# Kernel tuning notes

Hardware: AMD Instinct MI355X
Metric: run time of the kernel (lower is better)

## Reference

```python
import jax, jax.numpy as jnp
import numpy as np

E = 1024  # embedding_dim
H = 64    # head_size

def setup_inputs() -> dict:
    key = jax.random.key(0)
    k1, k2, k3, k4 = jax.random.split(key, 4)
    x = jax.random.normal(k1, (4, 4096, E), dtype=jnp.float32)
    # nn.Linear(E, H, bias=False) weights have shape [H, E]; y = x @ W.T
    s = 1.0 / np.sqrt(E)
    Wq = jax.random.normal(k2, (H, E), dtype=jnp.float32) * s
    Wk = jax.random.normal(k3, (H, E), dtype=jnp.float32) * s
    Wv = jax.random.normal(k4, (H, E), dtype=jnp.float32) * s
    return {"x": x, "Wq": Wq, "Wk": Wk, "Wv": Wv}

def reference(x, Wq, Wk, Wv):
    B, T, E_ = x.shape
    q = jnp.einsum('bte,he->bth', x, Wq)
    k = jnp.einsum('bte,he->bth', x, Wk)
    v = jnp.einsum('bte,he->bth', x, Wv)
    # NOTE: original scales by sqrt(embedding_dim), not head_size
    scores = jnp.einsum('bqh,bkh->bqk', q, k) / jnp.sqrt(jnp.asarray(E_, x.dtype))
    causal = jnp.tril(jnp.ones((T, T), dtype=bool))
    scores = jnp.where(causal, scores, -jnp.inf)
    weights = jax.nn.softmax(scores, axis=-1)
    return jnp.einsum('bqk,bkh->bqh', weights, v)
```

## Files before the change

### kernel.cpp

```cpp
#include <hip/hip_runtime.h>
#include <stdint.h>

typedef __bf16 bf16x8 __attribute__((ext_vector_type(8)));
typedef float  f32x4  __attribute__((ext_vector_type(4)));

#define E_DIM 1024
#define H_DIM 64
#define T_SEQ 4096
#define B_BAT 4
#define M_TOT (B_BAT * T_SEQ)

__device__ __forceinline__ uint32_t f2bf1(float f) {
    uint32_t u = __float_as_uint(f);
    return (u + 0x7FFFu + ((u >> 16) & 1u)) >> 16;
}
__device__ __forceinline__ uint32_t pk2(float lo, float hi) {
    return f2bf1(lo) | (f2bf1(hi) << 16);
}
__device__ __forceinline__ bf16x8 ldfrag(const ushort* p) {
    return __builtin_bit_cast(bf16x8, *(const uint4*)(p));
}
__device__ __forceinline__ void barrier_lgkm() {
    __builtin_amdgcn_s_waitcnt(0xC07F);
    __builtin_amdgcn_s_barrier();
}

__global__ __launch_bounds__(256) void wcvt(const float* __restrict__ Wq,
                                            const float* __restrict__ Wk,
                                            const float* __restrict__ Wv,
                                            ushort* __restrict__ Wfm) {
    int g = blockIdx.x * 256 + threadIdx.x;
    int n = g >> 7;
    int k8 = g & 127;
    const float* src = (n < 64) ? (Wq + (size_t)n * E_DIM)
                     : (n < 128) ? (Wk + (size_t)(n - 64) * E_DIM)
                     : (Wv + (size_t)(n - 128) * E_DIM);
    float sc = (n < 64) ? 0.03125f : 1.0f;
    float4 a = *(const float4*)(src + k8 * 8);
    float4 b = *(const float4*)(src + k8 * 8 + 4);
    uint4 o;
    o.x = pk2(a.x * sc, a.y * sc); o.y = pk2(a.z * sc, a.w * sc);
    o.z = pk2(b.x * sc, b.y * sc); o.w = pk2(b.z * sc, b.w * sc);
    int s = k8 >> 3, kc = (k8 >> 2) & 1, qd = k8 & 3;
    int nt = n >> 4, lm = n & 15;
    int lane = qd * 16 + lm;
    *(uint4*)(Wfm + (((size_t)(s * 12 + nt) * 2 + kc) * 64 + lane) * 8) = o;
}

__global__ __launch_bounds__(256, 3) void qkv(const float* __restrict__ x,
                                              const ushort* __restrict__ Wfm,
                                              ushort* __restrict__ Qfm,
                                              ushort* __restrict__ Kfm,
                                              ushort* __restrict__ Vfm) {
    __shared__ union {
        ushort a[2][32 * 72];
        struct { ushort c[32 * 136]; ushort vt[64 * 40]; } epi;
    } sm;
    const int tid = threadIdx.x;
    const int w = tid >> 6, l = tid & 63;
    const int lm = l & 15, qd = l >> 4;
    const int m0 = blockIdx.x * 32;

    f32x4 acc[2][3];
#pragma unroll
    for (int r2 = 0; r2 < 2; ++r2)
#pragma unroll
        for (int t = 0; t < 3; ++t) acc[r2][t] = (f32x4){0.f, 0.f, 0.f, 0.f};

    const int srow = tid >> 3, kseg = tid & 7;
    const float* xsrc = x + (size_t)(m0 + srow) * E_DIM + kseg * 8;

    {
        float4 a0 = *(const float4*)xsrc;
        float4 a1 = *(const float4*)(xsrc + 4);
        uint4 u = {pk2(a0.x, a0.y), pk2(a0.z, a0.w), pk2(a1.x, a1.y), pk2(a1.z, a1.w)};
        *(uint4*)(&sm.a[0][srow * 72 + kseg * 8]) = u;
    }
    float4 xn0 = *(const float4*)(xsrc + 64);
    float4 xn1 = *(const float4*)(xsrc + 68);
    __syncthreads();

    for (int s = 0; s < 16; ++s) {
        const int cb = s & 1, nb = cb ^ 1;
        float4 x20 = xn0, x21 = xn1;
        if (s < 14) {
            x20 = *(const float4*)(xsrc + (s + 2) * 64);
            x21 = *(const float4*)(xsrc + (s + 2) * 64 + 4);
        }
        bf16x8 wf[3][2];
#pragma unroll
        for (int t = 0; t < 3; ++t)
#pragma unroll
            for (int kc = 0; kc < 2; ++kc)
                wf[t][kc] = ldfrag(Wfm + (((size_t)(s * 12 + w * 3 + t) * 2 + kc) * 64 + l) * 8);
        bf16x8 af[2][2];
#pragma unroll
        for (int r2 = 0; r2 < 2; ++r2)
#pragma unroll
            for (int kc = 0; kc < 2; ++kc)
                af[r2][kc] = ldfrag(&sm.a[cb][(r2 * 16 + lm) * 72 + kc * 32 + qd * 8]);
#pragma unroll
        for (int t = 0; t < 3; ++t)
#pragma unroll
            for (int kc = 0; kc < 2; ++kc)
#pragma unroll
                for (int r2 = 0; r2 < 2; ++r2)
                    acc[r2][t] = __builtin_amdgcn_mfma_f32_16x16x32_bf16(af[r2][kc], wf[t][kc], acc[r2][t], 0, 0, 0);
        if (s < 15) {
            uint4 u = {pk2(xn0.x, xn0.y), pk2(xn0.z, xn0.w), pk2(xn1.x, xn1.y), pk2(xn1.z, xn1.w)};
            *(uint4*)(&sm.a[nb][srow * 72 + kseg * 8]) = u;
        }
        xn0 = x20; xn1 = x21;
        if (s < 15) barrier_lgkm();
    }
    __syncthreads();

#pragma unroll
    for (int r2 = 0; r2 < 2; ++r2)
#pragma unroll
        for (int t = 0; t < 3; ++t) {
            int gc = w * 48 + t * 16 + lm;
            int m = r2 * 16 + qd * 4;
#pragma unroll
            for (int rr = 0; rr < 4; ++rr) {
                ushort v = (ushort)f2bf1(acc[r2][t][rr]);
                if (gc < 128) sm.epi.c[(m + rr) * 136 + gc] = v;
                else          sm.epi.vt[(gc - 128) * 40 + (m + rr)] = v;
            }
        }
    __syncthreads();

    const int g16b = m0 >> 4;
    const int kt64 = m0 >> 6;
    const int tb   = (m0 >> 4) & 3;
    const int kcv  = (m0 >> 5) & 1;
#pragma unroll
    for (int ii = 0; ii < 3; ++ii) {
        int i = w + ii * 4;
        uint4 val;
        ushort* dst;
        if (i < 4) {
            int qt_l = i >> 1, kc = i & 1;
            val = *(const uint4*)(&sm.epi.c[(qt_l * 16 + lm) * 136 + kc * 32 + qd * 8]);
            dst = Qfm + (((size_t)(g16b + qt_l) * 2 + kc) * 64 + l) * 8;
        } else if (i < 8) {
            int j2 = i - 4, t_l = j2 >> 1, kc = j2 & 1;
            val = *(const uint4*)(&sm.epi.c[(t_l * 16 + lm) * 136 + 64 + kc * 32 + qd * 8]);
            dst = Kfm + (((size_t)((kt64 * 4 + tb + t_l) * 2 + kc)) * 64 + l) * 8;
        } else {
            int t = i - 8;
            val = *(const uint4*)(&sm.epi.vt[(t * 16 + lm) * 40 + qd * 8]);
            dst = Vfm + (((size_t)((kt64 * 4 + t) * 2 + kcv)) * 64 + l) * 8;
        }
        *(uint4*)dst = val;
    }
}

__global__ __launch_bounds__(256, 4) void flash(const ushort* __restrict__ Qfm,
                                                const ushort* __restrict__ Kfm,
                                                const ushort* __restrict__ Vfm,
                                                float* __restrict__ Opart,
                                                float* __restrict__ lpart) {
    __shared__ ushort plds[4][16 * 72];
    const int tid = threadIdx.x;
    const int wv = tid >> 6, l = tid & 63;
    const int lm = l & 15, qd = l >> 4;
    const int pr = blockIdx.x;
    const int bt = blockIdx.y;
    const int h  = blockIdx.z;
    ushort* myp = plds[wv];

#pragma unroll 1
    for (int half = 0; half < 2; ++half) {
        const int qt = half ? (63 - pr) : pr;
        const size_t rowg = (size_t)bt * T_SEQ + qt * 64 + wv * 16;
        const int g16 = bt * 256 + qt * 4 + wv;

        bf16x8 qf0, qf1;
        {
            const ushort* qp = Qfm + ((size_t)g16 * 2) * 512 + l * 8;
            qf0 = ldfrag(qp);
            qf1 = ldfrag(qp + 512);
        }
        f32x4 o[4];
#pragma unroll
        for (int t = 0; t < 4; ++t) o[t] = (f32x4){0.f, 0.f, 0.f, 0.f};
        float lacc = 0.f;

#pragma unroll 1
        for (int kt = h; kt <= qt; kt += 4) {
            const ushort* kb = Kfm + ((size_t)(bt * 64 + kt) * 8) * 512;
            const ushort* vb = Vfm + ((size_t)(bt * 64 + kt) * 8) * 512;
            f32x4 sf[4];
#pragma unroll
            for (int t = 0; t < 4; ++t) sf[t] = (f32x4){0.f, 0.f, 0.f, 0.f};
#pragma unroll
            for (int t = 0; t < 4; ++t) {
                bf16x8 k0 = ldfrag(kb + (t * 2 + 0) * 512 + l * 8);
                bf16x8 k1 = ldfrag(kb + (t * 2 + 1) * 512 + l * 8);
                sf[t] = __builtin_amdgcn_mfma_f32_16x16x32_bf16(k0, qf0, sf[t], 0, 0, 0);
                sf[t] = __builtin_amdgcn_mfma_f32_16x16x32_bf16(k1, qf1, sf[t], 0, 0, 0);
            }
            uint4 vu[4][2];
#pragma unroll
            for (int t = 0; t < 4; ++t) {
                vu[t][0] = *(const uint4*)(vb + (t * 2 + 0) * 512 + l * 8);
                vu[t][1] = *(const uint4*)(vb + (t * 2 + 1) * 512 + l * 8);
            }
            ushort* wp = myp + lm * 72 + qd * 4;
            if (kt != qt) {
#pragma unroll
                for (int t = 0; t < 4; ++t) {
                    float p0 = __expf(sf[t][0]), p1 = __expf(sf[t][1]);
                    float p2 = __expf(sf[t][2]), p3 = __expf(sf[t][3]);
                    lacc += (p0 + p1) + (p2 + p3);
                    *(uint2*)(wp + t * 16) = uint2{pk2(p0, p1), pk2(p2, p3)};
                }
            } else {
#pragma unroll
                for (int t = 0; t < 4; ++t) {
                    if (t < wv) {
                        float p0 = __expf(sf[t][0]), p1 = __expf(sf[t][1]);
                        float p2 = __expf(sf[t][2]), p3 = __expf(sf[t][3]);
                        lacc += (p0 + p1) + (p2 + p3);
                        *(uint2*)(wp + t * 16) = uint2{pk2(p0, p1), pk2(p2, p3)};
                    } else if (t == wv) {
                        float p[4];
#pragma unroll
                        for (int rr = 0; rr < 4; ++rr) {
                            float pe = __expf(sf[t][rr]);
                            if (qd * 4 + rr > lm) pe = 0.f;
                            lacc += pe;
                            p[rr] = pe;
                        }
                        *(uint2*)(wp + t * 16) = uint2{pk2(p[0], p[1]), pk2(p[2], p[3])};
                    } else {
                        *(uint2*)(wp + t * 16) = uint2{0u, 0u};
                    }
                }
            }
            __builtin_amdgcn_wave_barrier();
            __builtin_amdgcn_s_waitcnt(0xC07F);
            __builtin_amdgcn_wave_barrier();
            bf16x8 pf0 = ldfrag(myp + lm * 72 + qd * 8);
            bf16x8 pf1 = ldfrag(myp + lm * 72 + 32 + qd * 8);
#pragma unroll
            for (int t = 0; t < 4; ++t) {
                bf16x8 v0 = __builtin_bit_cast(bf16x8, vu[t][0]);
                bf16x8 v1 = __builtin_bit_cast(bf16x8, vu[t][1]);
                o[t] = __builtin_amdgcn_mfma_f32_16x16x32_bf16(pf0, v0, o[t], 0, 0, 0);
                o[t] = __builtin_amdgcn_mfma_f32_16x16x32_bf16(pf1, v1, o[t], 0, 0, 0);
            }
            __builtin_amdgcn_wave_barrier();
        }
        lacc += __shfl_xor(lacc, 16);
        lacc += __shfl_xor(lacc, 32);

        float* ob = Opart + ((size_t)h * M_TOT + rowg) * 64;
#pragma unroll
        for (int t = 0; t < 4; ++t)
#pragma unroll
            for (int rr = 0; rr < 4; ++rr)
                ob[(size_t)(qd * 4 + rr) * 64 + t * 16 + lm] = o[t][rr];
        if (qd == 0) lpart[(size_t)h * M_TOT + rowg + lm] = lacc;
    }
}

__global__ __launch_bounds__(256) void combine(const float* __restrict__ Opart,
                                               const float* __restrict__ lpart,
                                               float* __restrict__ out) {
    int i4 = blockIdx.x * 256 + threadIdx.x;
    size_t base = (size_t)i4 * 4;
    int row = i4 >> 4;
    float ls = lpart[row] + lpart[M_TOT + row] + lpart[2 * M_TOT + row] + lpart[3 * M_TOT + row];
    const size_t SP = (size_t)M_TOT * 64;
    float4 a = *(const float4*)(Opart + base);
    float4 b = *(const float4*)(Opart + SP + base);
    float4 c = *(const float4*)(Opart + 2 * SP + base);
    float4 d = *(const float4*)(Opart + 3 * SP + base);
    float inv = 1.0f / ls;
    float4 o;
    o.x = (a.x + b.x + c.x + d.x) * inv;
    o.y = (a.y + b.y + c.y + d.y) * inv;
    o.z = (a.z + b.z + c.z + d.z) * inv;
    o.w = (a.w + b.w + c.w + d.w) * inv;
    *(float4*)(out + base) = o;
}

extern "C" void kernel_launch(void* const* d_in, const int* in_sizes, int n_in,
                              void* d_out, int out_size, void* d_ws, size_t ws_size,
                              hipStream_t stream) {
    const float* x  = (const float*)d_in[0];
    const float* Wq = (const float*)d_in[1];
    const float* Wk = (const float*)d_in[2];
    const float* Wv = (const float*)d_in[3];
    float* out = (float*)d_out;

    char* ws = (char*)d_ws;
    ushort* Wfm = (ushort*)(ws);
    ushort* Qfm = (ushort*)(ws + 393216);
    ushort* Kfm = (ushort*)(ws + 2490368);
    ushort* Vfm = (ushort*)(ws + 4587520);
    float*  Op  = (float*) (ws + 6684672);
    float*  lp  = (float*) (ws + 23461888);

    wcvt<<<96, 256, 0, stream>>>(Wq, Wk, Wv, Wfm);
    qkv<<<512, 256, 0, stream>>>(x, Wfm, Qfm, Kfm, Vfm);
    flash<<<dim3(32, B_BAT, 4), 256, 0, stream>>>(Qfm, Kfm, Vfm, Op, lp);
    combine<<<1024, 256, 0, stream>>>(Op, lp, out);
}
```

Measured before the change: 135.8 us.

## Split key range eight ways, store partial outputs in bf16, use exp2

Doubles the key-dimension split in the flash kernel from 4 to 8, giving 1024 blocks and more parallelism for the causal workload. The partial outputs are stored as bf16 instead of fp32, which keeps the workspace size and the combine traffic in check while the combine kernel now sums 8 partials. The Q scale is folded with log2(e) so exp2f can replace __expf. The trade-offs are bf16 rounding of the partial sums, more lpart reads and more combine work. With the max-free softmax, larger exponents could also risk overflow.

After: 137.7 us. About the same (+1.4%).

```diff
diff --git a/kernel.cpp b/kernel.cpp
--- a/kernel.cpp
+++ b/kernel.cpp
@@ -9,6 +9,7 @@
 #define T_SEQ 4096
 #define B_BAT 4
 #define M_TOT (B_BAT * T_SEQ)
+#define NSPLIT 8
 
 __device__ __forceinline__ uint32_t f2bf1(float f) {
     uint32_t u = __float_as_uint(f);
@@ -19,6 +20,9 @@
 }
 __device__ __forceinline__ bf16x8 ldfrag(const ushort* p) {
     return __builtin_bit_cast(bf16x8, *(const uint4*)(p));
+}
+__device__ __forceinline__ float bf2f(uint32_t u) {
+    return __uint_as_float(u << 16);
 }
 __device__ __forceinline__ void barrier_lgkm() {
     __builtin_amdgcn_s_waitcnt(0xC07F);
@@ -35,7 +39,7 @@
     const float* src = (n < 64) ? (Wq + (size_t)n * E_DIM)
                      : (n < 128) ? (Wk + (size_t)(n - 64) * E_DIM)
                      : (Wv + (size_t)(n - 128) * E_DIM);
-    float sc = (n < 64) ? 0.03125f : 1.0f;
+    float sc = (n < 64) ? 0.04508422f : 1.0f;
     float4 a = *(const float4*)(src + k8 * 8);
     float4 b = *(const float4*)(src + k8 * 8 + 4);
     uint4 o;
@@ -159,7 +163,7 @@
 __global__ __launch_bounds__(256, 4) void flash(const ushort* __restrict__ Qfm,
                                                 const ushort* __restrict__ Kfm,
                                                 const ushort* __restrict__ Vfm,
-                                                float* __restrict__ Opart,
+                                                ushort* __restrict__ Opart,
                                                 float* __restrict__ lpart) {
     __shared__ ushort plds[4][16 * 72];
     const int tid = threadIdx.x;
@@ -188,7 +192,7 @@
         float lacc = 0.f;
 
 #pragma unroll 1
-        for (int kt = h; kt <= qt; kt += 4) {
+        for (int kt = h; kt <= qt; kt += NSPLIT) {
             const ushort* kb = Kfm + ((size_t)(bt * 64 + kt) * 8) * 512;
             const ushort* vb = Vfm + ((size_t)(bt * 64 + kt) * 8) * 512;
             f32x4 sf[4];
@@ -211,8 +215,8 @@
             if (kt != qt) {
 #pragma unroll
                 for (int t = 0; t < 4; ++t) {
-                    float p0 = __expf(sf[t][0]), p1 = __expf(sf[t][1]);
-                    float p2 = __expf(sf[t][2]), p3 = __expf(sf[t][3]);
+                    float p0 = exp2f(sf[t][0]), p1 = exp2f(sf[t][1]);
+                    float p2 = exp2f(sf[t][2]), p3 = exp2f(sf[t][3]);
                     lacc += (p0 + p1) + (p2 + p3);
                     *(uint2*)(wp + t * 16) = uint2{pk2(p0, p1), pk2(p2, p3)};
                 }
@@ -220,15 +224,15 @@
 #pragma unroll
                 for (int t = 0; t < 4; ++t) {
                     if (t < wv) {
-                        float p0 = __expf(sf[t][0]), p1 = __expf(sf[t][1]);
-                        float p2 = __expf(sf[t][2]), p3 = __expf(sf[t][3]);
+                        float p0 = exp2f(sf[t][0]), p1 = exp2f(sf[t][1]);
+                        float p2 = exp2f(sf[t][2]), p3 = exp2f(sf[t][3]);
                         lacc += (p0 + p1) + (p2 + p3);
                         *(uint2*)(wp + t * 16) = uint2{pk2(p0, p1), pk2(p2, p3)};
                     } else if (t == wv) {
                         float p[4];
 #pragma unroll
                         for (int rr = 0; rr < 4; ++rr) {
-                            float pe = __expf(sf[t][rr]);
+                            float pe = exp2f(sf[t][rr]);
                             if (qd * 4 + rr > lm) pe = 0.f;
                             lacc += pe;
                             p[rr] = pe;
@@ -256,34 +260,35 @@
         lacc += __shfl_xor(lacc, 16);
         lacc += __shfl_xor(lacc, 32);
 
-        float* ob = Opart + ((size_t)h * M_TOT + rowg) * 64;
+        ushort* ob = Opart + ((size_t)h * M_TOT + rowg) * 64;
 #pragma unroll
         for (int t = 0; t < 4; ++t)
 #pragma unroll
             for (int rr = 0; rr < 4; ++rr)
-                ob[(size_t)(qd * 4 + rr) * 64 + t * 16 + lm] = o[t][rr];
+                ob[(size_t)(qd * 4 + rr) * 64 + t * 16 + lm] = (ushort)f2bf1(o[t][rr]);
         if (qd == 0) lpart[(size_t)h * M_TOT + rowg + lm] = lacc;
     }
 }
 
-__global__ __launch_bounds__(256) void combine(const float* __restrict__ Opart,
+__global__ __launch_bounds__(256) void combine(const ushort* __restrict__ Opart,
                                                const float* __restrict__ lpart,
                                                float* __restrict__ out) {
     int i4 = blockIdx.x * 256 + threadIdx.x;
     size_t base = (size_t)i4 * 4;
     int row = i4 >> 4;
-    float ls = lpart[row] + lpart[M_TOT + row] + lpart[2 * M_TOT + row] + lpart[3 * M_TOT + row];
+    float ls = 0.f;
+#pragma unroll
+    for (int j = 0; j < NSPLIT; ++j) ls += lpart[(size_t)j * M_TOT + row];
+    float s0 = 0.f, s1 = 0.f, s2 = 0.f, s3 = 0.f;
     const size_t SP = (size_t)M_TOT * 64;
-    float4 a = *(const float4*)(Opart + base);
-    float4 b = *(const float4*)(Opart + SP + base);
-    float4 c = *(const float4*)(Opart + 2 * SP + base);
-    float4 d = *(const float4*)(Opart + 3 * SP + base);
+#pragma unroll
+    for (int j = 0; j < NSPLIT; ++j) {
+        uint2 u = *(const uint2*)(Opart + (size_t)j * SP + base);
+        s0 += bf2f(u.x & 0xFFFFu); s1 += bf2f(u.x >> 16);
+        s2 += bf2f(u.y & 0xFFFFu); s3 += bf2f(u.y >> 16);
+    }
     float inv = 1.0f / ls;
-    float4 o;
-    o.x = (a.x + b.x + c.x + d.x) * inv;
-    o.y = (a.y + b.y + c.y + d.y) * inv;
-    o.z = (a.z + b.z + c.z + d.z) * inv;
-    o.w = (a.w + b.w + c.w + d.w) * inv;
+    float4 o = {s0 * inv, s1 * inv, s2 * inv, s3 * inv};
     *(float4*)(out + base) = o;
 }
 
@@ -301,11 +306,11 @@
     ushort* Qfm = (ushort*)(ws + 393216);
     ushort* Kfm = (ushort*)(ws + 2490368);
     ushort* Vfm = (ushort*)(ws + 4587520);
-    float*  Op  = (float*) (ws + 6684672);
+    ushort* Op  = (ushort*)(ws + 6684672);
     float*  lp  = (float*) (ws + 23461888);
 
     wcvt<<<96, 256, 0, stream>>>(Wq, Wk, Wv, Wfm);
     qkv<<<512, 256, 0, stream>>>(x, Wfm, Qfm, Kfm, Vfm);
-    flash<<<dim3(32, B_BAT, 4), 256, 0, stream>>>(Qfm, Kfm, Vfm, Op, lp);
+    flash<<<dim3(32, B_BAT, NSPLIT), 256, 0, stream>>>(Qfm, Kfm, Vfm, Op, lp);
     combine<<<1024, 256, 0, stream>>>(Op, lp, out);
 }
```
